# Kernel optimization log

Measured on AMD Instinct MI355X. Metric: run time of the kernel, lower is better.

## Reference

```python
import jax, jax.numpy as jnp
import numpy as np

MASK_ATTENTION = 10000000000.0
PAD_IDX = 0


def setup_inputs() -> dict:
    key = jax.random.key(0)
    ks = jax.random.split(key, 12)
    S, T, B, H, V = 256, 64, 8, 768, 50257
    return {
        "encoder_out": jax.random.normal(ks[0], (S, B, H), dtype=jnp.float32),
        "decoder_state": jax.random.normal(ks[1], (T, B, H), dtype=jnp.float32),
        "src_ids": jax.random.randint(ks[2], (S, B), 0, V, dtype=jnp.int64),
        "tgt_embedding": jax.random.normal(ks[3], (T, B, H), dtype=jnp.float32),
        "W_attn": jax.random.normal(ks[4], (2 * H, H), dtype=jnp.float32) * 0.02,
        "b_attn": jax.random.normal(ks[5], (H,), dtype=jnp.float32) * 0.02,
        "v_attn": jax.random.normal(ks[6], (H,), dtype=jnp.float32) * 0.02,
        "b_v": jax.random.normal(ks[7], (1,), dtype=jnp.float32) * 0.02,
        "W_pgen": jax.random.normal(ks[8], (3 * H, 1), dtype=jnp.float32) * 0.02,
        "b_pgen": jax.random.normal(ks[9], (1,), dtype=jnp.float32) * 0.02,
        "W_gen": jax.random.normal(ks[10], (H, V), dtype=jnp.float32) * 0.02,
        "b_gen": jax.random.normal(ks[11], (V,), dtype=jnp.float32) * 0.02,
    }


def reference(encoder_out, decoder_state, src_ids, tgt_embedding,
              W_attn, b_attn, v_attn, b_v, W_pgen, b_pgen, W_gen, b_gen):
    # encoder_out: [S,B,H], decoder_state/tgt_embedding: [T,B,H], src_ids: [S,B]
    T, B, H = decoder_state.shape
    S = encoder_out.shape[0]
    # Split the cat+Linear into two projections (same math as Linear on concat)
    Wd, We = W_attn[:H], W_attn[H:]
    dec_proj = decoder_state @ Wd                     # [T,B,H]
    enc_proj = encoder_out @ We + b_attn              # [S,B,H]
    energy = jnp.tanh(dec_proj[:, None] + enc_proj[None])  # [T,S,B,H]
    attention = energy @ v_attn + b_v[0]              # [T,S,B]
    pad_mask = (src_ids == PAD_IDX)                   # [S,B]
    attn_dist = jnp.where(pad_mask[None], -MASK_ATTENTION, attention)
    attn_prob = jax.nn.softmax(attn_dist, axis=1)     # softmax over S: [T,S,B]
    ctx = jnp.einsum('tsb,sbh->tbh', attn_prob, encoder_out)  # [T,B,H]
    p_gen_input = jnp.concatenate((decoder_state, ctx, tgt_embedding), axis=2)
    p_gen = jax.nn.sigmoid(p_gen_input @ W_pgen + b_pgen)     # [T,B,1]
    vocab_prob = jax.nn.softmax(decoder_state @ W_gen + b_gen, axis=2)  # [T,B,V]
    vocab_prob_ = vocab_prob * p_gen
    attn_prob_ = jnp.transpose(attn_prob, (0, 2, 1)) * (1.0 - p_gen)    # [T,B,S]
    idx = jnp.broadcast_to(src_ids.T[None], (T, B, S))                  # [T,B,S]
    ti = jnp.arange(T)[:, None, None]
    bi = jnp.arange(B)[None, :, None]
    final_prob = vocab_prob_.at[ti, bi, idx].add(attn_prob_)
    return final_prob


if __name__ == "__main__":
    out = reference(**setup_inputs())
    print(out.shape)
```

## Files before the change

### kernel.cpp

```cpp
#include <hip/hip_runtime.h>
#include <stdint.h>

#define S_ 256
#define T_ 64
#define B_ 8
#define H_ 768
#define V_ 50257
#define R_ 512
#define VP_ 50304

typedef __attribute__((ext_vector_type(8))) short short8;
typedef __attribute__((ext_vector_type(4))) float float4v;

__device__ __forceinline__ float bf2f(unsigned short u) {
  union { unsigned int i; float f; } x; x.i = ((unsigned int)u) << 16; return x.f;
}
__device__ __forceinline__ short f2bf(float f) {
  union { float f; unsigned int i; } x; x.f = f;
  unsigned int u = x.i;
  unsigned int r = u + 0x7fffu + ((u >> 16) & 1u);
  return (short)(r >> 16);
}
__device__ __forceinline__ float tanh_fast(float x) {
  x = fminf(10.f, fmaxf(-10.f, x));
  float e = __expf(2.f * x);
  return (e - 1.f) * __builtin_amdgcn_rcpf(e + 1.f);
}
__device__ __forceinline__ void gload16(const short* g, short* l) {
  __builtin_amdgcn_global_load_lds(
      (const __attribute__((address_space(1))) unsigned int*)g,
      (__attribute__((address_space(3))) unsigned int*)l, 16, 0, 0);
}
__device__ __forceinline__ int swz(int r, int c) {
  return r * 64 + (c ^ ((r & 7) * 8));
}

__global__ __launch_bounds__(256) void cvt_kernel(const float* dec, const float* enc,
                                                  short* dec16, short* enc16, float* rowsums) {
  int i = blockIdx.x * 256 + threadIdx.x;
  if (i < R_) rowsums[i] = 0.f;
  const int nd = R_ * H_;
  if (i < nd) dec16[i] = f2bf(dec[i]);
  else        enc16[i - nd] = f2bf(enc[i - nd]);
}

__global__ __launch_bounds__(256) void twat_kernel(const float* in, short* out) {
  __shared__ float tile[64][65];
  int n0 = blockIdx.x * 64;
  int k0 = blockIdx.y * 64;
  int t = threadIdx.x;
  int c = t & 63, rsub = t >> 6;
#pragma unroll
  for (int i = 0; i < 16; ++i) {
    int r = i * 4 + rsub;
    tile[r][c] = in[(size_t)(k0 + r) * 768 + n0 + c];
  }
  __syncthreads();
#pragma unroll
  for (int i = 0; i < 16; ++i) {
    int nn = i * 4 + rsub;
    out[(size_t)(n0 + nn) * 1536 + k0 + c] = f2bf(tile[c][nn]);
  }
}

__global__ __launch_bounds__(256) void cvt_wt_kernel(const float* __restrict__ in,
                                                     short* __restrict__ out) {
  __shared__ float tile[64][65];
  int v0 = blockIdx.x * 64;
  int k0 = blockIdx.y * 64;
  int t = threadIdx.x;
  int c = t & 63, rsub = t >> 6;
#pragma unroll
  for (int i = 0; i < 16; ++i) {
    int r = i * 4 + rsub;
    int v = v0 + c;
    tile[r][c] = (v < V_) ? in[(size_t)(k0 + r) * V_ + v] : 0.f;
  }
  __syncthreads();
  int cp = t & 31, nsub = t >> 5;
#pragma unroll
  for (int i = 0; i < 8; ++i) {
    int nn = i * 8 + nsub;
    unsigned int pk = (unsigned int)(unsigned short)f2bf(tile[2 * cp][nn]) |
                      ((unsigned int)(unsigned short)f2bf(tile[2 * cp + 1][nn]) << 16);
    *(unsigned int*)&out[(size_t)(v0 + nn) * 768 + k0 + 2 * cp] = pk;
  }
}

__global__ __launch_bounds__(256) void gemm_proj(const short* __restrict__ A,
                                                 const short* __restrict__ BT,
                                                 int koff, const float* bias, float* C) {
  __shared__ short Al[128 * 32];
  __shared__ short Bl[64 * 32];
  int t = threadIdx.x;
  int w = t >> 6, l = t & 63;
  int m0 = blockIdx.y * 128, n0 = blockIdx.x * 64;
  int wm = w >> 1, wn = w & 1;
  float4v acc[4][2];
#pragma unroll
  for (int i = 0; i < 4; ++i)
#pragma unroll
    for (int j = 0; j < 2; ++j) acc[i][j] = float4v{0.f, 0.f, 0.f, 0.f};

#pragma unroll 1
  for (int kk = 0; kk < 768; kk += 32) {
#pragma unroll
    for (int i = 0; i < 2; ++i) {
      int q = t + i * 256;
      int m = q >> 2, k8 = (q & 3) * 8;
      *(short8*)&Al[m * 32 + k8] = *(const short8*)&A[(size_t)(m0 + m) * 768 + kk + k8];
    }
    {
      int n = t >> 2, k8 = (t & 3) * 8;
      *(short8*)&Bl[n * 32 + k8] = *(const short8*)&BT[(size_t)(n0 + n) * 1536 + koff + kk + k8];
    }
    __syncthreads();
    short8 af[4], bfr[2];
#pragma unroll
    for (int mt = 0; mt < 4; ++mt)
      af[mt] = *(short8*)&Al[(wm * 64 + mt * 16 + (l & 15)) * 32 + (l >> 4) * 8];
#pragma unroll
    for (int nt = 0; nt < 2; ++nt)
      bfr[nt] = *(short8*)&Bl[(wn * 32 + nt * 16 + (l & 15)) * 32 + (l >> 4) * 8];
#pragma unroll
    for (int mt = 0; mt < 4; ++mt)
#pragma unroll
      for (int nt = 0; nt < 2; ++nt)
        acc[mt][nt] = __builtin_amdgcn_mfma_f32_16x16x32_bf16(af[mt], bfr[nt], acc[mt][nt], 0, 0, 0);
    __syncthreads();
  }
  int q4 = (l >> 4) * 4, ln = l & 15;
#pragma unroll
  for (int nt = 0; nt < 2; ++nt) {
    int c = n0 + wn * 32 + nt * 16 + ln;
    float bv = bias ? bias[c] : 0.f;
#pragma unroll
    for (int mt = 0; mt < 4; ++mt)
#pragma unroll
      for (int r = 0; r < 4; ++r) {
        int row = m0 + wm * 64 + mt * 16 + q4 + r;
        C[(size_t)row * 768 + c] = acc[mt][nt][r] + bv;
      }
  }
}

__global__ __launch_bounds__(256) void energy_kernel(const float* __restrict__ dproj,
                                                     const float* __restrict__ eproj,
                                                     const float* vattn, const float* bv,
                                                     float* scores) {
  __shared__ float dch[16][65];
  __shared__ float ech[16][65];
  __shared__ float vch[64];
  int s0 = blockIdx.x * 16;
  int b  = blockIdx.y;
  int t0 = blockIdx.z * 16;
  int t = threadIdx.x;
  int sl = t & 15, tl = t >> 4;
  float acc = 0.f;
  for (int hc = 0; hc < 768; hc += 64) {
#pragma unroll
    for (int i = 0; i < 4; ++i) {
      int idx = i * 256 + t;
      int rr = idx >> 6, cc = idx & 63;
      dch[rr][cc] = dproj[(size_t)((t0 + rr) * 8 + b) * 768 + hc + cc];
      ech[rr][cc] = eproj[(size_t)((s0 + rr) * 8 + b) * 768 + hc + cc];
    }
    if (t < 64) vch[t] = vattn[hc + t];
    __syncthreads();
#pragma unroll 8
    for (int hh = 0; hh < 64; ++hh) {
      float x = dch[tl][hh] + ech[sl][hh];
      acc = fmaf(tanh_fast(x), vch[hh], acc);
    }
    __syncthreads();
  }
  scores[(size_t)((t0 + tl) * 8 + b) * 256 + s0 + sl] = acc + bv[0];
}

__global__ __launch_bounds__(256) void softmax_kernel(const float* scores, const int* sid, float* P) {
  __shared__ float red[256];
  int r = blockIdx.x, t = threadIdx.x, b = r & 7;
  float v = scores[(size_t)r * 256 + t];
  if (sid[t * 8 + b] == 0) v = -1e10f;
  red[t] = v;
  __syncthreads();
  for (int s = 128; s > 0; s >>= 1) {
    if (t < s) red[t] = fmaxf(red[t], red[t + s]);
    __syncthreads();
  }
  float m = red[0];
  __syncthreads();
  float e = __expf(v - m);
  red[t] = e;
  __syncthreads();
  for (int s = 128; s > 0; s >>= 1) {
    if (t < s) red[t] += red[t + s];
    __syncthreads();
  }
  P[(size_t)r * 256 + t] = e * (1.f / red[0]);
}

__global__ __launch_bounds__(256) void ctx_kernel(const float* __restrict__ P,
                                                  const float* __restrict__ enc, float* ctx) {
  __shared__ float Pl[16][256];
  int h0 = blockIdx.x * 64;
  int b  = blockIdx.y;
  int tg = blockIdx.z;
  int t = threadIdx.x;
  int hl = t & 63, wv = t >> 6;
#pragma unroll
  for (int i = 0; i < 16; ++i) {
    int idx = i * 256 + t;
    int tt = idx >> 8, s = idx & 255;
    Pl[tt][s] = P[(size_t)((tg * 16 + tt) * 8 + b) * 256 + s];
  }
  __syncthreads();
  float acc[4] = {0.f, 0.f, 0.f, 0.f};
#pragma unroll 4
  for (int s = 0; s < 256; ++s) {
    float e = enc[(size_t)(s * 8 + b) * 768 + h0 + hl];
#pragma unroll
    for (int j = 0; j < 4; ++j)
      acc[j] = fmaf(Pl[wv * 4 + j][s], e, acc[j]);
  }
#pragma unroll
  for (int j = 0; j < 4; ++j)
    ctx[(size_t)((tg * 16 + wv * 4 + j) * 8 + b) * 768 + h0 + hl] = acc[j];
}

__global__ __launch_bounds__(256) void pgen_kernel(const float* dec, const float* ctx,
                                                   const float* tgt, const float* Wp,
                                                   const float* bp, float* pgen) {
  __shared__ float red[256];
  int r = blockIdx.x, t = threadIdx.x;
  float s = 0.f;
  for (int h = t; h < 768; h += 256) {
    s = fmaf(dec[(size_t)r * 768 + h], Wp[h], s);
    s = fmaf(ctx[(size_t)r * 768 + h], Wp[768 + h], s);
    s = fmaf(tgt[(size_t)r * 768 + h], Wp[1536 + h], s);
  }
  red[t] = s;
  __syncthreads();
  for (int st = 128; st > 0; st >>= 1) {
    if (t < st) red[t] += red[t + st];
    __syncthreads();
  }
  if (t == 0) pgen[r] = 1.f / (1.f + __expf(-(red[0] + bp[0])));
}

__global__ __launch_bounds__(256) void gemm_vocab(const short* __restrict__ A,
                                                  const short* __restrict__ BT,
                                                  const float* __restrict__ bgen,
                                                  short* __restrict__ E, float* rowsums) {
  __shared__ __align__(16) short Al[2][128 * 64];
  __shared__ __align__(16) short Bl[2][128 * 64];
  int t = threadIdx.x;
  int w = t >> 6, l = t & 63;
  int bid = blockIdx.x;
  int n0 = (bid >> 2) * 128;
  int m0 = (bid & 3) * 128;
  int wm = w >> 1, wn = w & 1;
  int lm = l & 15, lq = l >> 4;
  int srow = t >> 3;
  int scol = ((t & 7) ^ (srow & 7)) * 8;

  float4v acc[4][4];
#pragma unroll
  for (int i = 0; i < 4; ++i)
#pragma unroll
    for (int j = 0; j < 4; ++j) acc[i][j] = float4v{0.f, 0.f, 0.f, 0.f};

  const short* aS = A  + (size_t)(m0 + srow) * 768 + scol;
  const short* bS = BT + (size_t)(n0 + srow) * 768 + scol;

  auto STAGE = [&](int buf, int kk) {
#pragma unroll
    for (int i = 0; i < 4; ++i) {
      gload16(aS + (size_t)i * 32 * 768 + kk, &Al[buf][(i * 32 + w * 8) * 64]);
      gload16(bS + (size_t)i * 32 * 768 + kk, &Bl[buf][(i * 32 + w * 8) * 64]);
    }
  };

  STAGE(0, 0);
#pragma unroll 1
  for (int kt = 0; kt < 12; ++kt) {
    int cb = kt & 1;
    if (kt < 11) {
      STAGE(cb ^ 1, (kt + 1) * 64);
      asm volatile("s_waitcnt vmcnt(8)" ::: "memory");
    } else {
      asm volatile("s_waitcnt vmcnt(0)" ::: "memory");
    }
    __builtin_amdgcn_s_barrier();

    short8 af[2][4], bfr[2][4];
#pragma unroll
    for (int ks = 0; ks < 2; ++ks) {
#pragma unroll
      for (int mt = 0; mt < 4; ++mt)
        af[ks][mt] = *(const short8*)&Al[cb][swz(wm * 64 + mt * 16 + lm, ks * 32 + lq * 8)];
#pragma unroll
      for (int nt = 0; nt < 4; ++nt)
        bfr[ks][nt] = *(const short8*)&Bl[cb][swz(wn * 64 + nt * 16 + lm, ks * 32 + lq * 8)];
    }
    asm volatile("s_waitcnt lgkmcnt(0)" ::: "memory");
    __builtin_amdgcn_s_barrier();

#pragma unroll
    for (int ks = 0; ks < 2; ++ks)
#pragma unroll
      for (int mt = 0; mt < 4; ++mt)
#pragma unroll
        for (int nt = 0; nt < 4; ++nt)
          acc[mt][nt] = __builtin_amdgcn_mfma_f32_16x16x32_bf16(af[ks][mt], bfr[ks][nt],
                                                                acc[mt][nt], 0, 0, 0);
  }

  int q4 = lq * 4, ln = lm;
  float rs[4][4];
#pragma unroll
  for (int i = 0; i < 4; ++i)
#pragma unroll
    for (int j = 0; j < 4; ++j) rs[i][j] = 0.f;
#pragma unroll
  for (int nt = 0; nt < 4; ++nt) {
    int c = n0 + wn * 64 + nt * 16 + ln;
    bool valid = c < V_;
    float bg = valid ? bgen[c] : 0.f;
#pragma unroll
    for (int mt = 0; mt < 4; ++mt)
#pragma unroll
      for (int r = 0; r < 4; ++r) {
        float e = valid ? __expf(acc[mt][nt][r] + bg) : 0.f;
        int row = m0 + wm * 64 + mt * 16 + q4 + r;
        E[(size_t)row * VP_ + c] = f2bf(e);
        rs[mt][r] += e;
      }
  }
#pragma unroll
  for (int mt = 0; mt < 4; ++mt)
#pragma unroll
    for (int r = 0; r < 4; ++r) {
      float v = rs[mt][r];
      v += __shfl_xor(v, 1);
      v += __shfl_xor(v, 2);
      v += __shfl_xor(v, 4);
      v += __shfl_xor(v, 8);
      if (ln == 0) atomicAdd(&rowsums[m0 + wm * 64 + mt * 16 + q4 + r], v);
    }
}

__global__ __launch_bounds__(256) void final_kernel(const short* __restrict__ E,
                                                    const float* __restrict__ P,
                                                    const float* pgen, const float* rowsums,
                                                    const int* sid, float* __restrict__ out) {
  int r = blockIdx.y, t = threadIdx.x, b = r & 7;
  int lo = blockIdx.x * 2048, hi = lo + 2048;
  float pg = pgen[r];
  float scale = pg / rowsums[r];
  const short* Er = E + (size_t)r * VP_;
  float* outr = out + (size_t)r * V_;
  int c0 = lo + t * 8;
  if (c0 < V_) {
    short8 ev = *(const short8*)&Er[c0];
#pragma unroll
    for (int j = 0; j < 8; ++j) {
      int c = c0 + j;
      if (c < V_) outr[c] = bf2f((unsigned short)ev[j]) * scale;
    }
  }
  __syncthreads();
  int idx = sid[t * 8 + b];
  if (idx >= lo && idx < hi) {
    float ap = (1.f - pg) * P[(size_t)r * 256 + t];
    atomicAdd(&outr[idx], ap);
  }
}

extern "C" void kernel_launch(void* const* d_in, const int* in_sizes, int n_in,
                              void* d_out, int out_size, void* d_ws, size_t ws_size,
                              hipStream_t stream) {
  const float* enc  = (const float*)d_in[0];
  const float* dec  = (const float*)d_in[1];
  const int*   sid  = (const int*)d_in[2];
  const float* tgt  = (const float*)d_in[3];
  const float* Wat  = (const float*)d_in[4];
  const float* batt = (const float*)d_in[5];
  const float* vatt = (const float*)d_in[6];
  const float* bv   = (const float*)d_in[7];
  const float* Wp   = (const float*)d_in[8];
  const float* bp   = (const float*)d_in[9];
  const float* Wg   = (const float*)d_in[10];
  const float* bg   = (const float*)d_in[11];
  float* out = (float*)d_out;

  char* ws = (char*)d_ws;
  size_t off = 0;
  auto alloc = [&](size_t bytes) -> char* {
    char* p = ws + off;
    off += (bytes + 255) & ~(size_t)255;
    return p;
  };
  short* E16     = (short*)alloc((size_t)R_ * VP_ * 2);
  short* WT16    = (short*)alloc((size_t)VP_ * H_ * 2);
  short* dec16   = (short*)alloc((size_t)R_ * H_ * 2);
  short* enc16   = (short*)alloc((size_t)S_ * B_ * H_ * 2);
  short* WAT16   = (short*)alloc((size_t)H_ * 1536 * 2);
  float* dproj   = (float*)alloc((size_t)R_ * H_ * 4);
  float* eproj   = (float*)alloc((size_t)S_ * B_ * H_ * 4);
  float* scores  = (float*)alloc((size_t)R_ * 256 * 4);
  float* P       = (float*)alloc((size_t)R_ * 256 * 4);
  float* ctx     = (float*)alloc((size_t)R_ * H_ * 4);
  float* pgen    = (float*)alloc(R_ * 4);
  float* rowsums = (float*)alloc(R_ * 4);

  cvt_kernel<<<7680, 256, 0, stream>>>(dec, enc, dec16, enc16, rowsums);
  twat_kernel<<<dim3(12, 24), 256, 0, stream>>>(Wat, WAT16);
  cvt_wt_kernel<<<dim3(786, 12), 256, 0, stream>>>(Wg, WT16);
  gemm_proj<<<dim3(12, 4), 256, 0, stream>>>(dec16, WAT16, 0, nullptr, dproj);
  gemm_proj<<<dim3(12, 16), 256, 0, stream>>>(enc16, WAT16, 768, batt, eproj);
  energy_kernel<<<dim3(16, 8, 4), 256, 0, stream>>>(dproj, eproj, vatt, bv, scores);
  softmax_kernel<<<512, 256, 0, stream>>>(scores, sid, P);
  ctx_kernel<<<dim3(12, 8, 4), 256, 0, stream>>>(P, enc, ctx);
  pgen_kernel<<<512, 256, 0, stream>>>(dec, ctx, tgt, Wp, bp, pgen);
  gemm_vocab<<<dim3(1572), 256, 0, stream>>>(dec16, WT16, bg, E16, rowsums);
  final_kernel<<<dim3(25, 512), 256, 0, stream>>>(E16, P, pgen, rowsums, sid, out);
}
```

Baseline: 598.9 us.

## Load A fragments directly to registers, remap blocks per XCD, raise occupancy

The vocab GEMM no longer stages the A (decoder-state) tile through LDS. Each wave now loads its A MFMA fragments straight from global memory into registers, which halves the LDS footprint and permits a launch bound of 3 blocks per CU. Block IDs are remapped so each XCD handles a contiguous range of tiles, aiming for better L2 reuse of the B (W_gen) tiles. The risk is extra global/L2 traffic, because A rows are re-read by every block and loaded in uncoalesced 16-byte pieces. The vmcnt wait counts are adjusted to match the new load mix.

```diff
diff --git a/kernel.cpp b/kernel.cpp
--- a/kernel.cpp
+++ b/kernel.cpp
@@ -248,17 +248,18 @@
   if (t == 0) pgen[r] = 1.f / (1.f + __expf(-(red[0] + bp[0])));
 }
 
-__global__ __launch_bounds__(256) void gemm_vocab(const short* __restrict__ A,
-                                                  const short* __restrict__ BT,
-                                                  const float* __restrict__ bgen,
-                                                  short* __restrict__ E, float* rowsums) {
-  __shared__ __align__(16) short Al[2][128 * 64];
+__global__ __launch_bounds__(256, 3) void gemm_vocab(const short* __restrict__ A,
+                                                     const short* __restrict__ BT,
+                                                     const float* __restrict__ bgen,
+                                                     short* __restrict__ E, float* rowsums) {
   __shared__ __align__(16) short Bl[2][128 * 64];
   int t = threadIdx.x;
   int w = t >> 6, l = t & 63;
-  int bid = blockIdx.x;
-  int n0 = (bid >> 2) * 128;
-  int m0 = (bid & 3) * 128;
+  int orig = blockIdx.x;
+  int xcd = orig & 7, ix = orig >> 3;
+  int wgid = (xcd < 4 ? xcd * 197 : 788 + (xcd - 4) * 196) + ix;
+  int n0 = (wgid >> 2) * 128;
+  int m0 = (wgid & 3) * 128;
   int wm = w >> 1, wn = w & 1;
   int lm = l & 15, lq = l >> 4;
   int srow = t >> 3;
@@ -270,40 +271,45 @@
 #pragma unroll
     for (int j = 0; j < 4; ++j) acc[i][j] = float4v{0.f, 0.f, 0.f, 0.f};
 
-  const short* aS = A  + (size_t)(m0 + srow) * 768 + scol;
   const short* bS = BT + (size_t)(n0 + srow) * 768 + scol;
+  const short* aR = A + (size_t)(m0 + wm * 64 + lm) * 768 + lq * 8;
 
   auto STAGE = [&](int buf, int kk) {
 #pragma unroll
-    for (int i = 0; i < 4; ++i) {
-      gload16(aS + (size_t)i * 32 * 768 + kk, &Al[buf][(i * 32 + w * 8) * 64]);
+    for (int i = 0; i < 4; ++i)
       gload16(bS + (size_t)i * 32 * 768 + kk, &Bl[buf][(i * 32 + w * 8) * 64]);
-    }
   };
 
   STAGE(0, 0);
 #pragma unroll 1
   for (int kt = 0; kt < 12; ++kt) {
     int cb = kt & 1;
+    int kk = kt * 64;
+    short8 af[2][4];
+#pragma unroll
+    for (int ks = 0; ks < 2; ++ks)
+#pragma unroll
+      for (int mt = 0; mt < 4; ++mt)
+        af[ks][mt] = *(const short8*)&aR[(size_t)mt * 16 * 768 + kk + ks * 32];
     if (kt < 11) {
-      STAGE(cb ^ 1, (kt + 1) * 64);
+      STAGE(cb ^ 1, kk + 64);
+      asm volatile("s_waitcnt vmcnt(12)" ::: "memory");
+    } else {
       asm volatile("s_waitcnt vmcnt(8)" ::: "memory");
-    } else {
-      asm volatile("s_waitcnt vmcnt(0)" ::: "memory");
     }
     __builtin_amdgcn_s_barrier();
 
-    short8 af[2][4], bfr[2][4];
-#pragma unroll
-    for (int ks = 0; ks < 2; ++ks) {
-#pragma unroll
-      for (int mt = 0; mt < 4; ++mt)
-        af[ks][mt] = *(const short8*)&Al[cb][swz(wm * 64 + mt * 16 + lm, ks * 32 + lq * 8)];
+    short8 bfr[2][4];
+#pragma unroll
+    for (int ks = 0; ks < 2; ++ks)
 #pragma unroll
       for (int nt = 0; nt < 4; ++nt)
         bfr[ks][nt] = *(const short8*)&Bl[cb][swz(wn * 64 + nt * 16 + lm, ks * 32 + lq * 8)];
-    }
     asm volatile("s_waitcnt lgkmcnt(0)" ::: "memory");
+    if (kt < 11)
+      asm volatile("s_waitcnt vmcnt(4)" ::: "memory");
+    else
+      asm volatile("s_waitcnt vmcnt(0)" ::: "memory");
     __builtin_amdgcn_s_barrier();
 
 #pragma unroll
```

Result: no change. 603.2 us (+0.7%).
